# Kernel tuning notes

Hardware: AMD Instinct MI355X
Metric: run time of the kernel (lower is better)

Reference implementation:

```python
import jax, jax.numpy as jnp
import numpy as np

C = 256      # in_channel
H = 8        # attention heads
B = 256      # number of graphs in the batch
S = 256      # max nodes per graph (dense batch length)
N = B * S - 100   # total nodes (last graph partially filled -> real padding mask)
E = 1_000_000     # total edges
EPS = 1e-5        # BatchNorm eps


def setup_inputs() -> dict:
    key = jax.random.key(0)
    ks = jax.random.split(key, 24)
    nrm = lambda k, shape: jax.random.normal(k, shape, jnp.float32) * 0.02
    x = jax.random.normal(ks[0], (N, C), jnp.float32)
    edge_index = jax.random.randint(ks[1], (2, E), 0, N)
    batch = jnp.minimum(jnp.arange(N) // S, B - 1)  # sorted graph ids, sizes <= S
    inp = {
        'x': x, 'edge_index': edge_index, 'batch': batch,
        # local GraphConv (PyG-style): W_root x_i + W_nei sum_j x_j + b_nei
        'W_root': nrm(ks[2], (C, C)), 'W_nei': nrm(ks[3], (C, C)), 'b_nei': jnp.zeros((C,), jnp.float32),
        # MultiheadAttention packed in/out projections
        'Wqkv': nrm(ks[4], (3 * C, C)), 'bqkv': jnp.zeros((3 * C,), jnp.float32),
        'Wo': nrm(ks[5], (C, C)), 'bo': jnp.zeros((C,), jnp.float32),
        # MLP: Linear(C,2C) -> ReLU -> Linear(2C,C)
        'W1': nrm(ks[6], (2 * C, C)), 'b1': jnp.zeros((2 * C,), jnp.float32),
        'W2': nrm(ks[7], (C, 2 * C)), 'b2': jnp.zeros((C,), jnp.float32),
    }
    # three BatchNorm1d layers (inference mode: running stats)
    for i, (kg, kv) in enumerate(((ks[8], ks[9]), (ks[10], ks[11]), (ks[12], ks[13])), start=1):
        inp[f'g{i}'] = 1.0 + nrm(kg, (C,))
        inp[f'be{i}'] = jnp.zeros((C,), jnp.float32)
        inp[f'm{i}'] = nrm(kv, (C,))
        inp[f'v{i}'] = jax.random.uniform(jax.random.fold_in(kv, 1), (C,), jnp.float32, 0.5, 1.5)
    return inp


def reference(x, edge_index, batch, W_root, W_nei, b_nei, Wqkv, bqkv, Wo, bo,
              W1, b1, W2, b2, g1, be1, m1, v1, g2, be2, m2, v2, g3, be3, m3, v3):
    def bn(h, g, b, m, v):
        return (h - m) * (g * jax.lax.rsqrt(v + EPS)) + b

    # --- local message passing conv + residual + BN (dropout = identity, eval) ---
    src, dst = edge_index[0], edge_index[1]
    agg = jax.ops.segment_sum(x[src], dst, num_segments=N)        # [N, C]
    h = agg @ W_nei.T + b_nei + x @ W_root.T
    h1 = bn(h + x, g1, be1, m1, v1)

    # --- to_dense_batch(x, batch) ---
    counts = jax.ops.segment_sum(jnp.ones((N,), jnp.int32), batch, num_segments=B)
    starts = jnp.concatenate([jnp.zeros((1,), jnp.int32), jnp.cumsum(counts)[:-1].astype(jnp.int32)])
    pos = jnp.arange(N) - starts[batch]                            # position within graph
    dense = jnp.zeros((B, S, C), x.dtype).at[batch, pos].set(x)    # [B, S, C]
    mask = jnp.zeros((B, S), bool).at[batch, pos].set(True)

    # --- MultiheadAttention(dense, dense, dense, key_padding_mask=~mask) ---
    qkv = dense @ Wqkv.T + bqkv
    q, k, v = jnp.split(qkv, 3, axis=-1)
    Dh = C // H
    q = q.reshape(B, S, H, Dh)
    k = k.reshape(B, S, H, Dh)
    v = v.reshape(B, S, H, Dh)
    scores = jnp.einsum('bqhd,bkhd->bhqk', q, k) / jnp.sqrt(jnp.float32(Dh))
    scores = jnp.where(mask[:, None, None, :], scores, jnp.float32(-1e9))
    probs = jax.nn.softmax(scores, axis=-1)
    attn = jnp.einsum('bhqk,bkhd->bqhd', probs, v).reshape(B, S, C)
    attn = attn @ Wo.T + bo

    # gather back h[mask] (row-major order == node order since batch is sorted)
    h2 = bn(attn[batch, pos] + x, g2, be2, m2, v2)

    # --- sum of branches + residual MLP + BN ---
    out = h1 + h2
    mlp = jax.nn.relu(out @ W1.T + b1) @ W2.T + b2
    return bn(out + mlp, g3, be3, m3, v3)
```

## Files before the change

### kernel.cpp

```cpp
#include <hip/hip_runtime.h>
#include <hip/hip_bf16.h>

typedef __attribute__((ext_vector_type(8))) short bf16x8;
typedef __attribute__((ext_vector_type(4))) short bf16x4;
typedef __attribute__((ext_vector_type(4))) float f32x4;
typedef unsigned short u16;
typedef unsigned int u32;

#define BN_EPS 1e-5f
#define NBINS 65536

__device__ __forceinline__ float b2f(u16 u) {
    u32 x = ((u32)u) << 16;
    float f; __builtin_memcpy(&f, &x, 4); return f;
}
__device__ __forceinline__ u16 f2b(float f) {
    f = fminf(fmaxf(f, -3.0e38f), 3.0e38f);
    __hip_bfloat16 h = __float2bfloat16(f);
    u16 s; __builtin_memcpy(&s, &h, 2); return s;
}
__device__ __forceinline__ bf16x8 cvt8(f32x4 a, f32x4 b) {
    bf16x8 r;
    r[0] = (short)f2b(a[0]); r[1] = (short)f2b(a[1]);
    r[2] = (short)f2b(a[2]); r[3] = (short)f2b(a[3]);
    r[4] = (short)f2b(b[0]); r[5] = (short)f2b(b[1]);
    r[6] = (short)f2b(b[2]); r[7] = (short)f2b(b[3]);
    return r;
}
#define MFMA(a, b, c) __builtin_amdgcn_mfma_f32_16x16x32_bf16((a), (b), (c), 0, 0, 0)

#if __has_builtin(__builtin_amdgcn_mfma_f32_16x16x16bf16_1k)
__device__ __forceinline__ f32x4 mfma16(bf16x4 a, bf16x4 b, f32x4 c) {
    return __builtin_amdgcn_mfma_f32_16x16x16bf16_1k(a, b, c, 0, 0, 0);
}
#else
__device__ __forceinline__ f32x4 mfma16(bf16x4 a, bf16x4 b, f32x4 c) {
    asm volatile("v_mfma_f32_16x16x16_bf16 %0, %1, %2, %0"
                 : "+v"(c) : "v"(a), "v"(b));
    return c;
}
#endif

__global__ __launch_bounds__(256) void k_cvtw(const float* __restrict__ src,
                                              u16* __restrict__ dst, int n) {
    const int i = blockIdx.x * 256 + threadIdx.x;
    if (i < n) dst[i] = f2b(src[i]);
}
__global__ __launch_bounds__(256) void k_cvtx(const float* __restrict__ src,
                                              u16* __restrict__ dst, int n4) {
    const int i = blockIdx.x * 256 + threadIdx.x;
    if (i < n4) {
        const f32x4 v = ((const f32x4*)src)[i];
        ushort4 pk;
        pk.x = f2b(v[0]); pk.y = f2b(v[1]); pk.z = f2b(v[2]); pk.w = f2b(v[3]);
        ((ushort4*)dst)[i] = pk;
    }
}

__global__ __launch_bounds__(256) void k_hist(
    const int* __restrict__ edst, int* __restrict__ counts, int E) {
    const int i = blockIdx.x * 256 + threadIdx.x;
    if (i < E) atomicAdd(&counts[edst[i]], 1);
}

__global__ __launch_bounds__(1024) void k_scan(
    const int* __restrict__ counts, int* __restrict__ start,
    int* __restrict__ cursor) {
    __shared__ int sums[1024];
    const int t = threadIdx.x;
    const int base = t * 64;
    int s = 0;
#pragma unroll 8
    for (int j = 0; j < 64; ++j) s += counts[base + j];
    sums[t] = s;
    __syncthreads();
    for (int off = 1; off < 1024; off <<= 1) {
        const int tmp = (t >= off) ? sums[t - off] : 0;
        __syncthreads();
        sums[t] += tmp;
        __syncthreads();
    }
    int run = sums[t] - s;
    for (int j = 0; j < 64; ++j) {
        start[base + j] = run;
        cursor[base + j] = run;
        run += counts[base + j];
    }
    if (t == 1023) start[NBINS] = run;
}

__global__ __launch_bounds__(256) void k_reorder(
    const int* __restrict__ esrc, const int* __restrict__ edst,
    int* __restrict__ cursor, int* __restrict__ ssrc, int E) {
    const int i = blockIdx.x * 256 + threadIdx.x;
    if (i < E) {
        const int p = atomicAdd(&cursor[edst[i]], 1);
        ssrc[p] = esrc[i];
    }
}

__global__ __launch_bounds__(256) void k_aggregate(
    const u16* __restrict__ xb, const int* __restrict__ ssrc,
    const int* __restrict__ start, u16* __restrict__ agg,
    int lo, int hi) {
    const int rel = (blockIdx.x << 2) + (threadIdx.x >> 6);
    const int r = lo + rel;
    if (r >= hi) return;
    const int lane = threadIdx.x & 63;
    const int s0 = start[r], s1 = start[r + 1];
    f32x4 acc = {0.f, 0.f, 0.f, 0.f};
    int j = s0;
    int sNext = (j < s1) ? ssrc[j] : 0;
    while (j < s1) {
        const int s = sNext;
        ++j;
        if (j < s1) sNext = ssrc[j];
        const ushort4 xv = *(const ushort4*)(xb + (size_t)s * 256 + lane * 4);
        acc[0] += b2f(xv.x); acc[1] += b2f(xv.y);
        acc[2] += b2f(xv.z); acc[3] += b2f(xv.w);
    }
    ushort4 pk;
    pk.x = f2b(acc[0]); pk.y = f2b(acc[1]); pk.z = f2b(acc[2]); pk.w = f2b(acc[3]);
    *(ushort4*)(agg + (size_t)rel * 256 + lane * 4) = pk;
}

template<bool ABF16>
__device__ __forceinline__ void gemm_acc(const void* A, int lda, int Mload,
                                         const u16* W, int K,
                                         int rowBase, int colBase,
                                         f32x4 (&acc)[2][4])
{
    const int lane = threadIdx.x & 63;
    const int r16 = lane & 15;
    const int quad = lane >> 4;
    int r0 = rowBase + r16;
    int r1 = rowBase + 16 + r16;
    const bool z0 = (r0 >= Mload), z1 = (r1 >= Mload);
    if (z0) r0 = 0;
    if (z1) r1 = 0;
    const bf16x8 zf = {0,0,0,0,0,0,0,0};
    for (int kk = 0; kk < K; kk += 32) {
        const int ko = kk + quad * 8;
        bf16x8 a0, a1;
        if (ABF16) {
            const u16* Ab = (const u16*)A;
            a0 = *(const bf16x8*)(Ab + (size_t)r0 * lda + ko);
            a1 = *(const bf16x8*)(Ab + (size_t)r1 * lda + ko);
        } else {
            const float* Af = (const float*)A;
            const f32x4* p0 = (const f32x4*)(Af + (size_t)r0 * lda + ko);
            const f32x4* p1 = (const f32x4*)(Af + (size_t)r1 * lda + ko);
            a0 = cvt8(p0[0], p0[1]);
            a1 = cvt8(p1[0], p1[1]);
        }
        if (z0) a0 = zf;
        if (z1) a1 = zf;
#pragma unroll
        for (int nt = 0; nt < 4; ++nt) {
            const bf16x8 b = *(const bf16x8*)(W + (size_t)(colBase + nt * 16 + r16) * K + ko);
            acc[0][nt] = MFMA(a0, b, acc[0][nt]);
            acc[1][nt] = MFMA(a1, b, acc[1][nt]);
        }
    }
}

__global__ __launch_bounds__(256) void k_attn(
    const u16* __restrict__ xb, const u16* __restrict__ Wqkv,
    const float* __restrict__ bqkv, u16* __restrict__ attnOut,
    int lo, int N, int ngraph)
{
    __shared__ u16 ks_s[256 * 40];
    __shared__ u16 vt_s[32 * 264];
    int brel, h;
    if ((ngraph & 7) == 0) {
        const int x8 = blockIdx.x & 7;
        const int j  = blockIdx.x >> 3;
        h = j & 7;
        brel = x8 + 8 * (j >> 3);
    } else {
        brel = blockIdx.x >> 3;
        h = blockIdx.x & 7;
    }
    const int base = lo + brel * 256;
    const int count = min(256, N - base);
    const int t = threadIdx.x;
    const int wave = t >> 6;
    const int lane = t & 63;
    const int r16 = lane & 15;
    const int quad = lane >> 4;
    u16* qsc = ks_s + wave * 64 * 40;
    const float scale = 0.17677669529663687f;

    bf16x8 qa[4];

#pragma unroll
    for (int sel = 0; sel < 3; ++sel) {
        f32x4 acc[4][2] = {};
        for (int kk = 0; kk < 256; kk += 32) {
            const int ko = kk + quad * 8;
            bf16x8 a[4];
#pragma unroll
            for (int mt = 0; mt < 4; ++mt) {
                int row = base + wave * 64 + mt * 16 + r16;
                row = min(row, N - 1);
                a[mt] = *(const bf16x8*)(xb + (size_t)row * 256 + ko);
            }
#pragma unroll
            for (int nt = 0; nt < 2; ++nt) {
                const int wrow = sel * 256 + h * 32 + nt * 16 + r16;
                const bf16x8 b = *(const bf16x8*)(Wqkv + (size_t)wrow * 256 + ko);
#pragma unroll
                for (int mt = 0; mt < 4; ++mt)
                    acc[mt][nt] = MFMA(a[mt], b, acc[mt][nt]);
            }
        }
        if (sel == 0) {
#pragma unroll
            for (int nt = 0; nt < 2; ++nt) {
                const float bias = bqkv[h * 32 + nt * 16 + r16];
#pragma unroll
                for (int mt = 0; mt < 4; ++mt)
#pragma unroll
                    for (int r = 0; r < 4; ++r)
                        qsc[(mt * 16 + quad * 4 + r) * 40 + nt * 16 + r16] =
                            f2b((acc[mt][nt][r] + bias) * scale);
            }
#pragma unroll
            for (int mt = 0; mt < 4; ++mt)
                qa[mt] = *(const bf16x8*)(qsc + (mt * 16 + r16) * 40 + quad * 8);
        } else if (sel == 1) {
#pragma unroll
            for (int nt = 0; nt < 2; ++nt) {
                const float bias = bqkv[256 + h * 32 + nt * 16 + r16];
#pragma unroll
                for (int mt = 0; mt < 4; ++mt)
#pragma unroll
                    for (int r = 0; r < 4; ++r) {
                        const int key = wave * 64 + mt * 16 + quad * 4 + r;
                        ks_s[key * 40 + nt * 16 + r16] = f2b(acc[mt][nt][r] + bias);
                    }
            }
        } else {
#pragma unroll
            for (int nt = 0; nt < 2; ++nt) {
                const int d = nt * 16 + r16;
                const float bias = bqkv[512 + h * 32 + d];
#pragma unroll
                for (int mt = 0; mt < 4; ++mt) {
                    const int key0 = wave * 64 + mt * 16 + quad * 4;
                    ushort4 pk;
                    pk.x = f2b(acc[mt][nt][0] + bias);
                    pk.y = f2b(acc[mt][nt][1] + bias);
                    pk.z = f2b(acc[mt][nt][2] + bias);
                    pk.w = f2b(acc[mt][nt][3] + bias);
                    *(ushort4*)(vt_s + d * 264 + key0) = pk;
                }
            }
        }
    }
    __syncthreads();

#pragma unroll
    for (int mp = 0; mp < 2; ++mp) {
        f32x4 O[2][2] = {};
        float rs2[2] = {0.f, 0.f};
        for (int kb = 0; kb < 8; ++kb) {
            bf16x8 bk[2];
#pragma unroll
            for (int kt = 0; kt < 2; ++kt)
                bk[kt] = *(const bf16x8*)(ks_s + (kb * 32 + kt * 16 + r16) * 40 + quad * 8);
            f32x4 st[2][2];
#pragma unroll
            for (int kt = 0; kt < 2; ++kt)
#pragma unroll
                for (int mt = 0; mt < 2; ++mt) {
                    const f32x4 z = {0.f, 0.f, 0.f, 0.f};
                    st[kt][mt] = MFMA(bk[kt], qa[mp * 2 + mt], z);
                }
            bf16x4 pf[2][2];
#pragma unroll
            for (int kt = 0; kt < 2; ++kt) {
                const int key0 = kb * 32 + kt * 16 + quad * 4;
#pragma unroll
                for (int mt = 0; mt < 2; ++mt) {
                    bf16x4 p;
#pragma unroll
                    for (int r = 0; r < 4; ++r) {
                        const float s = fminf(fmaxf(st[kt][mt][r], -60.f), 60.f);
                        const float e = (key0 + r < count) ? __expf(s) : 0.f;
                        rs2[mt] += e;
                        p[r] = (short)f2b(e);
                    }
                    pf[kt][mt] = p;
                }
            }
            bf16x4 bv[2][2];
#pragma unroll
            for (int kt = 0; kt < 2; ++kt)
#pragma unroll
                for (int ntd = 0; ntd < 2; ++ntd)
                    bv[kt][ntd] = *(const bf16x4*)(vt_s + (ntd * 16 + r16) * 264
                                                   + kb * 32 + kt * 16 + quad * 4);
#pragma unroll
            for (int kt = 0; kt < 2; ++kt)
#pragma unroll
                for (int mt = 0; mt < 2; ++mt)
#pragma unroll
                    for (int ntd = 0; ntd < 2; ++ntd)
                        O[mt][ntd] = mfma16(pf[kt][mt], bv[kt][ntd], O[mt][ntd]);
        }
#pragma unroll
        for (int mt = 0; mt < 2; ++mt) {
            float v = rs2[mt];
            v += __shfl_xor(v, 16, 64);
            v += __shfl_xor(v, 32, 64);
            rs2[mt] = v;
        }
#pragma unroll
        for (int mt = 0; mt < 2; ++mt) {
#pragma unroll
            for (int r = 0; r < 4; ++r) {
                const float rsv = __shfl(rs2[mt], quad * 4 + r, 16);
                const float inv = 1.f / fmaxf(rsv, 1e-30f);
                const int qrow = wave * 64 + mp * 32 + mt * 16 + quad * 4 + r;
#pragma unroll
                for (int ntd = 0; ntd < 2; ++ntd)
                    attnOut[(size_t)(brel * 256 + qrow) * 256 + h * 32 + ntd * 16 + r16]
                        = f2b(O[mt][ntd][r] * inv);
            }
        }
    }
}

__global__ __launch_bounds__(256) void k_hout(
    const u16* __restrict__ attn, const u16* __restrict__ agg,
    const u16* __restrict__ xbc, const float* __restrict__ x,
    const u16* __restrict__ Wo, const float* __restrict__ bo,
    const u16* __restrict__ Wnei, const u16* __restrict__ Wroot,
    const float* __restrict__ bnei,
    const float* __restrict__ g1, const float* __restrict__ be1,
    const float* __restrict__ m1, const float* __restrict__ v1,
    const float* __restrict__ g2, const float* __restrict__ be2,
    const float* __restrict__ m2, const float* __restrict__ v2,
    float* __restrict__ dout, int lo, int hi)
{
    const int wave = threadIdx.x >> 6;
    const int rowBase = blockIdx.y * 128 + wave * 32;
    const int colBase = blockIdx.x * 64;
    const int ML = hi - lo;
    f32x4 accC[2][4] = {};
    f32x4 accA[2][4] = {};
    gemm_acc<true>(agg, 256, ML, Wnei, 256, rowBase, colBase, accC);
    gemm_acc<true>(xbc, 256, ML, Wroot, 256, rowBase, colBase, accC);
    gemm_acc<true>(attn, 256, ML, Wo, 256, rowBase, colBase, accA);
    const int lane = threadIdx.x & 63;
    const int r16 = lane & 15, quad = lane >> 4;
#pragma unroll
    for (int nt = 0; nt < 4; ++nt) {
        const int col = colBase + nt * 16 + r16;
        const float b1v = bnei[col];
        const float mm1 = m1[col];
        const float sc1 = g1[col] * rsqrtf(v1[col] + BN_EPS);
        const float bb1 = be1[col];
        const float b2v = bo[col];
        const float mm2 = m2[col];
        const float sc2 = g2[col] * rsqrtf(v2[col] + BN_EPS);
        const float bb2 = be2[col];
#pragma unroll
        for (int tt = 0; tt < 2; ++tt) {
#pragma unroll
            for (int r = 0; r < 4; ++r) {
                const int rel = rowBase + tt * 16 + quad * 4 + r;
                if (rel < ML) {
                    const size_t idx = (size_t)(lo + rel) * 256 + col;
                    const float xv = x[idx];
                    const float h1 = (accC[tt][nt][r] + b1v + xv - mm1) * sc1 + bb1;
                    const float h2 = (accA[tt][nt][r] + b2v + xv - mm2) * sc2 + bb2;
                    dout[idx] = h1 + h2;
                }
            }
        }
    }
}

__global__ __launch_bounds__(256) void k_mlp(
    const u16* __restrict__ W1, const float* __restrict__ b1,
    const u16* __restrict__ W2, const float* __restrict__ b2v,
    const float* __restrict__ g3, const float* __restrict__ be3,
    const float* __restrict__ m3, const float* __restrict__ v3,
    float* __restrict__ dout, int N)
{
    __shared__ u16 as[64 * 264];
    __shared__ u16 ts[64 * 136];
    const int rowBase = blockIdx.x * 64;
    const int t = threadIdx.x;
    const int wave = t >> 6;
    const int lane = t & 63;
    const int r16 = lane & 15;
    const int quad = lane >> 4;

#pragma unroll
    for (int i = t; i < 64 * 64; i += 256) {
        const int row = i >> 6;
        const int c4 = i & 63;
        int grow = rowBase + row;
        grow = min(grow, N - 1);
        const f32x4 v = *(const f32x4*)(dout + (size_t)grow * 256 + c4 * 4);
        ushort4 pk;
        pk.x = f2b(v[0]); pk.y = f2b(v[1]); pk.z = f2b(v[2]); pk.w = f2b(v[3]);
        *(ushort4*)(as + row * 264 + c4 * 4) = pk;
    }
    __syncthreads();

    f32x4 yacc[4][4] = {};

    for (int s = 0; s < 4; ++s) {
        f32x4 a1[4][2] = {};
        for (int kk = 0; kk < 256; kk += 32) {
            const int ko = kk + quad * 8;
            bf16x8 a[4];
#pragma unroll
            for (int mt = 0; mt < 4; ++mt)
                a[mt] = *(const bf16x8*)(as + (mt * 16 + r16) * 264 + ko);
#pragma unroll
            for (int nt = 0; nt < 2; ++nt) {
                const int wrow = s * 128 + wave * 32 + nt * 16 + r16;
                const bf16x8 b = *(const bf16x8*)(W1 + (size_t)wrow * 256 + ko);
#pragma unroll
                for (int mt = 0; mt < 4; ++mt)
                    a1[mt][nt] = MFMA(a[mt], b, a1[mt][nt]);
            }
        }
        __syncthreads();
#pragma unroll
        for (int nt = 0; nt < 2; ++nt) {
            const int col = wave * 32 + nt * 16 + r16;
            const float bias = b1[s * 128 + col];
#pragma unroll
            for (int mt = 0; mt < 4; ++mt) {
#pragma unroll
                for (int r = 0; r < 4; ++r) {
                    const int row = mt * 16 + quad * 4 + r;
                    ts[row * 136 + col] = f2b(fmaxf(a1[mt][nt][r] + bias, 0.f));
                }
            }
        }
        __syncthreads();
        for (int kk = 0; kk < 128; kk += 32) {
            const int ko = kk + quad * 8;
            bf16x8 a[4];
#pragma unroll
            for (int mt = 0; mt < 4; ++mt)
                a[mt] = *(const bf16x8*)(ts + (mt * 16 + r16) * 136 + ko);
#pragma unroll
            for (int nt = 0; nt < 4; ++nt) {
                const int wrow = wave * 64 + nt * 16 + r16;
                const bf16x8 b = *(const bf16x8*)(W2 + (size_t)wrow * 512 + s * 128 + ko);
#pragma unroll
                for (int mt = 0; mt < 4; ++mt)
                    yacc[mt][nt] = MFMA(a[mt], b, yacc[mt][nt]);
            }
        }
    }
#pragma unroll
    for (int nt = 0; nt < 4; ++nt) {
        const int col = wave * 64 + nt * 16 + r16;
        const float bias = b2v[col];
        const float mm = m3[col];
        const float sc = g3[col] * rsqrtf(v3[col] + BN_EPS);
        const float bb = be3[col];
#pragma unroll
        for (int mt = 0; mt < 4; ++mt) {
#pragma unroll
            for (int r = 0; r < 4; ++r) {
                const int grow = rowBase + mt * 16 + quad * 4 + r;
                if (grow < N) {
                    const size_t idx = (size_t)grow * 256 + col;
                    const float val = yacc[mt][nt][r] + bias + dout[idx];
                    dout[idx] = (val - mm) * sc + bb;
                }
            }
        }
    }
}

extern "C" void kernel_launch(void* const* d_in, const int* in_sizes, int n_in,
                              void* d_out, int out_size, void* d_ws, size_t ws_size,
                              hipStream_t stream)
{
    (void)n_in; (void)out_size;
    const int N = in_sizes[0] / 256;
    const int E = in_sizes[1] / 2;

    const float* x     = (const float*)d_in[0];
    const int*   ei    = (const int*)d_in[1];
    const float* Wroot = (const float*)d_in[3];
    const float* Wnei  = (const float*)d_in[4];
    const float* bnei  = (const float*)d_in[5];
    const float* Wqkv  = (const float*)d_in[6];
    const float* bqkv  = (const float*)d_in[7];
    const float* Wo    = (const float*)d_in[8];
    const float* bo    = (const float*)d_in[9];
    const float* W1    = (const float*)d_in[10];
    const float* b1    = (const float*)d_in[11];
    const float* W2    = (const float*)d_in[12];
    const float* b2    = (const float*)d_in[13];
    const float* g1 = (const float*)d_in[14], *be1 = (const float*)d_in[15];
    const float* m1 = (const float*)d_in[16], *v1  = (const float*)d_in[17];
    const float* g2 = (const float*)d_in[18], *be2 = (const float*)d_in[19];
    const float* m2 = (const float*)d_in[20], *v2  = (const float*)d_in[21];
    const float* g3 = (const float*)d_in[22], *be3 = (const float*)d_in[23];
    const float* m3 = (const float*)d_in[24], *v3  = (const float*)d_in[25];
    float* dout = (float*)d_out;

    u16* wb = (u16*)d_ws;
    u16* Wroot_b = wb;
    u16* Wnei_b  = wb + 65536;
    u16* Wqkv_b  = wb + 131072;
    u16* Wo_b    = wb + 327680;
    u16* W1_b    = wb + 393216;
    u16* W2_b    = wb + 524288;
    const size_t WB_BYTES   = 2u << 20;
    const size_t META_BYTES = 1u << 20;
    const size_t SORT_BYTES = 4u << 20;
    const size_t XB_BYTES   = 32u << 20;
    const size_t FIXED = WB_BYTES + META_BYTES + SORT_BYTES + XB_BYTES;

    int* meta   = (int*)((char*)d_ws + WB_BYTES);
    int* counts = meta;
    int* start  = meta + NBINS;
    int* cursor = start + NBINS + 1;
    int* ssrc   = (int*)((char*)d_ws + WB_BYTES + META_BYTES);
    u16* xb     = (u16*)((char*)d_ws + WB_BYTES + META_BYTES + SORT_BYTES);

    k_cvtw<<<dim3(256),  256, 0, stream>>>(Wroot, Wroot_b, 65536);
    k_cvtw<<<dim3(256),  256, 0, stream>>>(Wnei,  Wnei_b,  65536);
    k_cvtw<<<dim3(768),  256, 0, stream>>>(Wqkv,  Wqkv_b,  196608);
    k_cvtw<<<dim3(256),  256, 0, stream>>>(Wo,    Wo_b,    65536);
    k_cvtw<<<dim3(512),  256, 0, stream>>>(W1,    W1_b,    131072);
    k_cvtw<<<dim3(512),  256, 0, stream>>>(W2,    W2_b,    131072);
    const int n4 = (N * 256) / 4;
    k_cvtx<<<dim3((n4 + 255) / 256), 256, 0, stream>>>(x, xb, n4);

    size_t arena = (ws_size > FIXED) ? (ws_size - FIXED) : 0;
    size_t maxRows = arena / 1024;
    int chunkRows = (int)((maxRows < 65536 ? maxRows : 65536) & ~(size_t)255);
    if (chunkRows < 256) chunkRows = 256;

    u16* agg  = (u16*)((char*)d_ws + FIXED);
    u16* attn = agg + (size_t)chunkRows * 256;

    hipMemsetAsync(counts, 0, NBINS * 4, stream);
    k_hist   <<<dim3((E + 255) / 256), 256, 0, stream>>>(ei + E, counts, E);
    k_scan   <<<dim3(1), 1024, 0, stream>>>(counts, start, cursor);
    k_reorder<<<dim3((E + 255) / 256), 256, 0, stream>>>(ei, ei + E, cursor, ssrc, E);

    for (int lo = 0; lo < N; lo += chunkRows) {
        const int hi = min(lo + chunkRows, N);
        const int ngraph = (hi - lo + 255) / 256;
        k_aggregate<<<dim3((hi - lo + 3) / 4), 256, 0, stream>>>(xb, ssrc, start, agg, lo, hi);
        k_attn<<<dim3(ngraph * 8), 256, 0, stream>>>(xb, Wqkv_b, bqkv, attn, lo, N, ngraph);
        k_hout<<<dim3(4, (hi - lo + 127) / 128), 256, 0, stream>>>(
            attn, agg, xb + (size_t)lo * 256, x,
            Wo_b, bo, Wnei_b, Wroot_b, bnei,
            g1, be1, m1, v1, g2, be2, m2, v2, dout, lo, hi);
    }
    k_mlp<<<dim3((N + 63) / 64), 256, 0, stream>>>(
        W1_b, b1, W2_b, b2, g3, be3, m3, v3, dout, N);
}
```

Measured before the change: 820.2 us.

## Fold BatchNorm scales into weights and merge prep kernels

Fold the BN1/BN2/BN3 per-channel scales into the bf16 weights (Wroot, Wnei, Wo, W2) and precompute combined bias and residual-scale vectors. This lets k_hout use a single accumulator and widen each block to 128 output columns. The six weight-conversion launches and the counts memset are merged into one prep kernel. Folding the scale before bf16 rounding changes rounding slightly, and the wider tile doubles the accumulator registers, which may reduce occupancy.

```diff
diff --git a/kernel.cpp b/kernel.cpp
--- a/kernel.cpp
+++ b/kernel.cpp
@@ -41,11 +41,56 @@
 }
 #endif
 
-__global__ __launch_bounds__(256) void k_cvtw(const float* __restrict__ src,
-                                              u16* __restrict__ dst, int n) {
+__global__ __launch_bounds__(256) void k_prep(
+    const float* __restrict__ Wroot, const float* __restrict__ Wnei,
+    const float* __restrict__ Wqkv,  const float* __restrict__ Wo,
+    const float* __restrict__ W1,    const float* __restrict__ W2,
+    const float* __restrict__ bnei,  const float* __restrict__ bo,
+    const float* __restrict__ b2,
+    const float* __restrict__ g1, const float* __restrict__ be1,
+    const float* __restrict__ m1, const float* __restrict__ v1,
+    const float* __restrict__ g2, const float* __restrict__ be2,
+    const float* __restrict__ m2, const float* __restrict__ v2,
+    const float* __restrict__ g3, const float* __restrict__ be3,
+    const float* __restrict__ m3, const float* __restrict__ v3,
+    u16* __restrict__ wb, int* __restrict__ counts, float* __restrict__ fvec)
+{
     const int i = blockIdx.x * 256 + threadIdx.x;
-    if (i < n) dst[i] = f2b(src[i]);
-}
+    if (i < 655360) {
+        float v;
+        if (i < 65536) {
+            const int col = i >> 8;
+            v = Wroot[i] * (g1[col] * rsqrtf(v1[col] + BN_EPS));
+        } else if (i < 131072) {
+            const int j = i - 65536, col = j >> 8;
+            v = Wnei[j] * (g1[col] * rsqrtf(v1[col] + BN_EPS));
+        } else if (i < 327680) {
+            v = Wqkv[i - 131072];
+        } else if (i < 393216) {
+            const int j = i - 327680, col = j >> 8;
+            v = Wo[j] * (g2[col] * rsqrtf(v2[col] + BN_EPS));
+        } else if (i < 524288) {
+            v = W1[i - 393216];
+        } else {
+            const int j = i - 524288, col = j >> 9;
+            v = W2[j] * (g3[col] * rsqrtf(v3[col] + BN_EPS));
+        }
+        wb[i] = f2b(v);
+    } else if (i < 720896) {
+        counts[i - 655360] = 0;
+    } else if (i < 721152) {
+        const int col = i - 720896;
+        const float sc1 = g1[col] * rsqrtf(v1[col] + BN_EPS);
+        const float sc2 = g2[col] * rsqrtf(v2[col] + BN_EPS);
+        const float sc3 = g3[col] * rsqrtf(v3[col] + BN_EPS);
+        fvec[col]       = sc1 * (bnei[col] - m1[col]) + be1[col]
+                        + sc2 * (bo[col]  - m2[col]) + be2[col];
+        fvec[256 + col] = sc1 + sc2;
+        fvec[512 + col] = sc3 * (b2[col] - m3[col]) + be3[col];
+        fvec[768 + col] = sc3;
+    }
+}
+
 __global__ __launch_bounds__(256) void k_cvtx(const float* __restrict__ src,
                                               u16* __restrict__ dst, int n4) {
     const int i = blockIdx.x * 256 + threadIdx.x;
@@ -124,11 +169,11 @@
     *(ushort4*)(agg + (size_t)rel * 256 + lane * 4) = pk;
 }
 
-template<bool ABF16>
-__device__ __forceinline__ void gemm_acc(const void* A, int lda, int Mload,
-                                         const u16* W, int K,
-                                         int rowBase, int colBase,
-                                         f32x4 (&acc)[2][4])
+template<int NT>
+__device__ __forceinline__ void gemm_accN(const u16* A, int lda, int Mload,
+                                          const u16* W, int K,
+                                          int rowBase, int colBase,
+                                          f32x4 (&acc)[2][NT])
 {
     const int lane = threadIdx.x & 63;
     const int r16 = lane & 15;
@@ -141,22 +186,12 @@
     const bf16x8 zf = {0,0,0,0,0,0,0,0};
     for (int kk = 0; kk < K; kk += 32) {
         const int ko = kk + quad * 8;
-        bf16x8 a0, a1;
-        if (ABF16) {
-            const u16* Ab = (const u16*)A;
-            a0 = *(const bf16x8*)(Ab + (size_t)r0 * lda + ko);
-            a1 = *(const bf16x8*)(Ab + (size_t)r1 * lda + ko);
-        } else {
-            const float* Af = (const float*)A;
-            const f32x4* p0 = (const f32x4*)(Af + (size_t)r0 * lda + ko);
-            const f32x4* p1 = (const f32x4*)(Af + (size_t)r1 * lda + ko);
-            a0 = cvt8(p0[0], p0[1]);
-            a1 = cvt8(p1[0], p1[1]);
-        }
+        bf16x8 a0 = *(const bf16x8*)(A + (size_t)r0 * lda + ko);
+        bf16x8 a1 = *(const bf16x8*)(A + (size_t)r1 * lda + ko);
         if (z0) a0 = zf;
         if (z1) a1 = zf;
 #pragma unroll
-        for (int nt = 0; nt < 4; ++nt) {
+        for (int nt = 0; nt < NT; ++nt) {
             const bf16x8 b = *(const bf16x8*)(W + (size_t)(colBase + nt * 16 + r16) * K + ko);
             acc[0][nt] = MFMA(a0, b, acc[0][nt]);
             acc[1][nt] = MFMA(a1, b, acc[1][nt]);
@@ -335,37 +370,25 @@
 __global__ __launch_bounds__(256) void k_hout(
     const u16* __restrict__ attn, const u16* __restrict__ agg,
     const u16* __restrict__ xbc, const float* __restrict__ x,
-    const u16* __restrict__ Wo, const float* __restrict__ bo,
-    const u16* __restrict__ Wnei, const u16* __restrict__ Wroot,
-    const float* __restrict__ bnei,
-    const float* __restrict__ g1, const float* __restrict__ be1,
-    const float* __restrict__ m1, const float* __restrict__ v1,
-    const float* __restrict__ g2, const float* __restrict__ be2,
-    const float* __restrict__ m2, const float* __restrict__ v2,
+    const u16* __restrict__ Wo, const u16* __restrict__ Wnei,
+    const u16* __restrict__ Wroot, const float* __restrict__ fvec,
     float* __restrict__ dout, int lo, int hi)
 {
     const int wave = threadIdx.x >> 6;
     const int rowBase = blockIdx.y * 128 + wave * 32;
-    const int colBase = blockIdx.x * 64;
+    const int colBase = blockIdx.x * 128;
     const int ML = hi - lo;
-    f32x4 accC[2][4] = {};
-    f32x4 accA[2][4] = {};
-    gemm_acc<true>(agg, 256, ML, Wnei, 256, rowBase, colBase, accC);
-    gemm_acc<true>(xbc, 256, ML, Wroot, 256, rowBase, colBase, accC);
-    gemm_acc<true>(attn, 256, ML, Wo, 256, rowBase, colBase, accA);
+    f32x4 acc[2][8] = {};
+    gemm_accN<8>(agg, 256, ML, Wnei, 256, rowBase, colBase, acc);
+    gemm_accN<8>(xbc, 256, ML, Wroot, 256, rowBase, colBase, acc);
+    gemm_accN<8>(attn, 256, ML, Wo, 256, rowBase, colBase, acc);
     const int lane = threadIdx.x & 63;
     const int r16 = lane & 15, quad = lane >> 4;
 #pragma unroll
-    for (int nt = 0; nt < 4; ++nt) {
+    for (int nt = 0; nt < 8; ++nt) {
         const int col = colBase + nt * 16 + r16;
-        const float b1v = bnei[col];
-        const float mm1 = m1[col];
-        const float sc1 = g1[col] * rsqrtf(v1[col] + BN_EPS);
-        const float bb1 = be1[col];
-        const float b2v = bo[col];
-        const float mm2 = m2[col];
-        const float sc2 = g2[col] * rsqrtf(v2[col] + BN_EPS);
-        const float bb2 = be2[col];
+        const float cb = fvec[col];
+        const float xs = fvec[256 + col];
 #pragma unroll
         for (int tt = 0; tt < 2; ++tt) {
 #pragma unroll
@@ -373,10 +396,7 @@
                 const int rel = rowBase + tt * 16 + quad * 4 + r;
                 if (rel < ML) {
                     const size_t idx = (size_t)(lo + rel) * 256 + col;
-                    const float xv = x[idx];
-                    const float h1 = (accC[tt][nt][r] + b1v + xv - mm1) * sc1 + bb1;
-                    const float h2 = (accA[tt][nt][r] + b2v + xv - mm2) * sc2 + bb2;
-                    dout[idx] = h1 + h2;
+                    dout[idx] = acc[tt][nt][r] + xs * x[idx] + cb;
                 }
             }
         }
@@ -385,9 +405,7 @@
 
 __global__ __launch_bounds__(256) void k_mlp(
     const u16* __restrict__ W1, const float* __restrict__ b1,
-    const u16* __restrict__ W2, const float* __restrict__ b2v,
-    const float* __restrict__ g3, const float* __restrict__ be3,
-    const float* __restrict__ m3, const float* __restrict__ v3,
+    const u16* __restrict__ W2, const float* __restrict__ fvec,
     float* __restrict__ dout, int N)
 {
     __shared__ u16 as[64 * 264];
@@ -465,10 +483,8 @@
 #pragma unroll
     for (int nt = 0; nt < 4; ++nt) {
         const int col = wave * 64 + nt * 16 + r16;
-        const float bias = b2v[col];
-        const float mm = m3[col];
-        const float sc = g3[col] * rsqrtf(v3[col] + BN_EPS);
-        const float bb = be3[col];
+        const float cb3 = fvec[512 + col];
+        const float xs3 = fvec[768 + col];
 #pragma unroll
         for (int mt = 0; mt < 4; ++mt) {
 #pragma unroll
@@ -476,8 +492,7 @@
                 const int grow = rowBase + mt * 16 + quad * 4 + r;
                 if (grow < N) {
                     const size_t idx = (size_t)grow * 256 + col;
-                    const float val = yacc[mt][nt][r] + bias + dout[idx];
-                    dout[idx] = (val - mm) * sc + bb;
+                    dout[idx] = yacc[mt][nt][r] + xs3 * dout[idx] + cb3;
                 }
             }
         }
@@ -520,6 +535,7 @@
     u16* Wo_b    = wb + 327680;
     u16* W1_b    = wb + 393216;
     u16* W2_b    = wb + 524288;
+    float* fvec  = (float*)(wb + 655360);
     const size_t WB_BYTES   = 2u << 20;
     const size_t META_BYTES = 1u << 20;
     const size_t SORT_BYTES = 4u << 20;
@@ -533,12 +549,10 @@
     int* ssrc   = (int*)((char*)d_ws + WB_BYTES + META_BYTES);
     u16* xb     = (u16*)((char*)d_ws + WB_BYTES + META_BYTES + SORT_BYTES);
 
-    k_cvtw<<<dim3(256),  256, 0, stream>>>(Wroot, Wroot_b, 65536);
-    k_cvtw<<<dim3(256),  256, 0, stream>>>(Wnei,  Wnei_b,  65536);
-    k_cvtw<<<dim3(768),  256, 0, stream>>>(Wqkv,  Wqkv_b,  196608);
-    k_cvtw<<<dim3(256),  256, 0, stream>>>(Wo,    Wo_b,    65536);
-    k_cvtw<<<dim3(512),  256, 0, stream>>>(W1,    W1_b,    131072);
-    k_cvtw<<<dim3(512),  256, 0, stream>>>(W2,    W2_b,    131072);
+    k_prep<<<dim3(2817), 256, 0, stream>>>(
+        Wroot, Wnei, Wqkv, Wo, W1, W2, bnei, bo, b2,
+        g1, be1, m1, v1, g2, be2, m2, v2, g3, be3, m3, v3,
+        wb, counts, fvec);
     const int n4 = (N * 256) / 4;
     k_cvtx<<<dim3((n4 + 255) / 256), 256, 0, stream>>>(x, xb, n4);
 
@@ -550,7 +564,6 @@
     u16* agg  = (u16*)((char*)d_ws + FIXED);
     u16* attn = agg + (size_t)chunkRows * 256;
 
-    hipMemsetAsync(counts, 0, NBINS * 4, stream);
     k_hist   <<<dim3((E + 255) / 256), 256, 0, stream>>>(ei + E, counts, E);
     k_scan   <<<dim3(1), 1024, 0, stream>>>(counts, start, cursor);
     k_reorder<<<dim3((E + 255) / 256), 256, 0, stream>>>(ei, ei + E, cursor, ssrc, E);
@@ -560,11 +573,10 @@
         const int ngraph = (hi - lo + 255) / 256;
         k_aggregate<<<dim3((hi - lo + 3) / 4), 256, 0, stream>>>(xb, ssrc, start, agg, lo, hi);
         k_attn<<<dim3(ngraph * 8), 256, 0, stream>>>(xb, Wqkv_b, bqkv, attn, lo, N, ngraph);
-        k_hout<<<dim3(4, (hi - lo + 127) / 128), 256, 0, stream>>>(
+        k_hout<<<dim3(2, (hi - lo + 127) / 128), 256, 0, stream>>>(
             attn, agg, xb + (size_t)lo * 256, x,
-            Wo_b, bo, Wnei_b, Wroot_b, bnei,
-            g1, be1, m1, v1, g2, be2, m2, v2, dout, lo, hi);
+            Wo_b, Wnei_b, Wroot_b, fvec, dout, lo, hi);
     }
     k_mlp<<<dim3((N + 63) / 64), 256, 0, stream>>>(
-        W1_b, b1, W2_b, b2, g3, be3, m3, v3, dout, N);
-}
+        W1_b, b1, W2_b, fvec, dout, N);
+}
```

New measurement: 835.2 us. Within noise of the previous version (+1.8%).
